# Performance work log

Hardware: AMD Instinct MI355X
Metric: run time of the kernel (lower is better)

## Reference

```python
import jax, jax.numpy as jnp
import numpy as np

DIM = 512
NUM_HEADS = 8
DIM_HEAD = 64
EPS = 1e-8
ROPE_THETA = 10000.0


def rms_norm(x, gamma):
    # F.normalize(x, dim=-1, p=2, eps) * sqrt(dim) * gamma
    norm = jnp.sqrt(jnp.sum(x * x, axis=-1, keepdims=True))
    x = x / jnp.maximum(norm, EPS)
    return x * (DIM ** 0.5) * gamma


def apply_rope(x):
    # x: [b, h, n, d], interleaved-pair RoPE (rotary-embedding-torch style)
    n, d = x.shape[-2], x.shape[-1]
    inv_freq = 1.0 / (ROPE_THETA ** (jnp.arange(0, d, 2, dtype=jnp.float32) / d))
    freqs = jnp.arange(n, dtype=jnp.float32)[:, None] * inv_freq[None, :]  # [n, d/2]
    freqs = jnp.repeat(freqs, 2, axis=-1)  # [n, d]
    cos, sin = jnp.cos(freqs), jnp.sin(freqs)
    x1 = x[..., ::2]
    x2 = x[..., 1::2]
    rot = jnp.stack((-x2, x1), axis=-1).reshape(x.shape)
    return x * cos + rot * sin


def setup_inputs() -> dict:
    key = jax.random.key(0)
    k1, k2, k3, k4 = jax.random.split(key, 4)
    b, n = 4, 2048
    dim_inner = NUM_HEADS * DIM_HEAD
    x = jax.random.normal(k1, (b, n, DIM), dtype=jnp.float32)
    gamma = jnp.ones((DIM,), dtype=jnp.float32)
    w_qkv = jax.random.normal(k2, (DIM, 3 * dim_inner), dtype=jnp.float32) * (DIM ** -0.5)
    w_out = jax.random.normal(k3, (dim_inner, DIM), dtype=jnp.float32) * (dim_inner ** -0.5)
    return {"x": x, "gamma": gamma, "w_qkv": w_qkv, "w_out": w_out}


def reference(x, gamma, w_qkv, w_out):
    b, n, _ = x.shape
    h, d = NUM_HEADS, DIM_HEAD
    xn = rms_norm(x, gamma)
    qkv = xn @ w_qkv  # [b, n, 3*h*d]
    qkv = qkv.reshape(b, n, 3, h, d)
    q = jnp.transpose(qkv[:, :, 0], (0, 2, 1, 3))  # [b, h, n, d]
    k = jnp.transpose(qkv[:, :, 1], (0, 2, 1, 3))
    v = jnp.transpose(qkv[:, :, 2], (0, 2, 1, 3))
    q = apply_rope(q)
    k = apply_rope(k)
    scale = d ** -0.5
    attn = jnp.einsum('bhnd,bhmd->bhnm', q, k) * scale
    attn = jax.nn.softmax(attn, axis=-1)
    out = jnp.einsum('bhnm,bhmd->bhnd', attn, v)
    out = jnp.transpose(out, (0, 2, 1, 3)).reshape(b, n, h * d)
    return out @ w_out
```

## Files before the change

### kernel.cpp

```cpp
#include <hip/hip_runtime.h>
#include <hip/hip_bf16.h>
#include <cmath>

#define B_SZ 4
#define N_SEQ 2048
#define DIM 512
#define NH 8
#define DH 64
#define QKV_N 1536
#define ROWS (B_SZ * N_SEQ)

typedef __bf16 bf16x8 __attribute__((ext_vector_type(8)));
typedef __bf16 bf16x4 __attribute__((ext_vector_type(4)));
typedef float  f32x4  __attribute__((ext_vector_type(4)));

#define GLOAD_LDS16(gp, lp)                                                     \
    __builtin_amdgcn_global_load_lds(                                           \
        (const __attribute__((address_space(1))) void*)(gp),                    \
        (__attribute__((address_space(3))) void*)(lp), 16, 0, 0)

#define MFMA_BF16 __builtin_amdgcn_mfma_f32_16x16x32_bf16

__global__ __launch_bounds__(64) void rmscast_kernel(const float* __restrict__ x,
                                                     const float* __restrict__ gamma,
                                                     __bf16* __restrict__ A) {
    int row = blockIdx.x;
    int t = threadIdx.x;
    const float4* xr = (const float4*)(x + (size_t)row * DIM);
    float4 a = xr[t];
    float4 b = xr[t + 64];
    float ss = a.x*a.x + a.y*a.y + a.z*a.z + a.w*a.w
             + b.x*b.x + b.y*b.y + b.z*b.z + b.w*b.w;
    #pragma unroll
    for (int off = 32; off > 0; off >>= 1) ss += __shfl_xor(ss, off, 64);
    float s = 22.62741699796952f / fmaxf(sqrtf(ss), 1e-8f);
    const float4* gr = (const float4*)gamma;
    float4 g1 = gr[t], g2 = gr[t + 64];
    bf16x4 o1 = { (__bf16)(a.x*g1.x*s), (__bf16)(a.y*g1.y*s),
                  (__bf16)(a.z*g1.z*s), (__bf16)(a.w*g1.w*s) };
    bf16x4 o2 = { (__bf16)(b.x*g2.x*s), (__bf16)(b.y*g2.y*s),
                  (__bf16)(b.z*g2.z*s), (__bf16)(b.w*g2.w*s) };
    *(bf16x4*)(A + (size_t)row * DIM + t * 4)       = o1;
    *(bf16x4*)(A + (size_t)row * DIM + 256 + t * 4) = o2;
}

__device__ __forceinline__ void tcast_tile(const float* __restrict__ W,
                                           __bf16* __restrict__ Wt,
                                           int K, int N, int n0, int k0, int t,
                                           float (*Ls)[68]) {
    const int tx = t & 15, ty = t >> 4;
    #pragma unroll
    for (int i = 0; i < 4; i++) {
        int k = ty + i * 16;
        float4 v = *(const float4*)&W[(size_t)(k0 + k) * N + n0 + tx * 4];
        *(float4*)&Ls[k][tx * 4] = v;
    }
    __syncthreads();
    const int nrow = t >> 2, seg = (t & 3) * 16;
    bf16x8 o0, o1;
    #pragma unroll
    for (int j = 0; j < 8; j++) o0[j] = (__bf16)Ls[seg + j][nrow];
    #pragma unroll
    for (int j = 0; j < 8; j++) o1[j] = (__bf16)Ls[seg + 8 + j][nrow];
    *(bf16x8*)&Wt[(size_t)(n0 + nrow) * K + k0 + seg]     = o0;
    *(bf16x8*)&Wt[(size_t)(n0 + nrow) * K + k0 + seg + 8] = o1;
}

__global__ __launch_bounds__(256) void tcast2_kernel(const float* __restrict__ w_qkv,
                                                     const float* __restrict__ w_out,
                                                     __bf16* __restrict__ Wqkvt,
                                                     __bf16* __restrict__ Woutt) {
    __shared__ float Ls[64][68];
    const int bx = blockIdx.x, k0 = blockIdx.y * 64, t = threadIdx.x;
    if (bx < 24) tcast_tile(w_qkv, Wqkvt, DIM, QKV_N, bx * 64, k0, t, Ls);
    else         tcast_tile(w_out, Woutt, DIM, DIM, (bx - 24) * 64, k0, t, Ls);
}

template <int N, typename OutT>
__global__ __launch_bounds__(256) void gemm_bf16_kernel(const __bf16* __restrict__ A,
                                                        const __bf16* __restrict__ Bt,
                                                        OutT* __restrict__ C) {
    __shared__ __bf16 As[128 * 32];
    __shared__ __bf16 Bs[128 * 32];
    const int t = threadIdx.x;
    const int lane = t & 63;
    const int w = t >> 6;
    const int l16 = lane & 15, quad = lane >> 4;
    const int wr = w >> 1, wc = w & 1;
    const int row0 = blockIdx.y * 128, col0 = blockIdx.x * 128;

    f32x4 acc[4][4] = {};

    const int r0a = t >> 2,         ks0 = (t & 3) * 8;
    const int r1a = (t + 256) >> 2, ks1 = (t & 3) * 8;

    for (int kt = 0; kt < DIM; kt += 32) {
        __syncthreads();
        GLOAD_LDS16(A  + (size_t)(row0 + r0a) * DIM + kt + ks0, As + t * 8);
        GLOAD_LDS16(A  + (size_t)(row0 + r1a) * DIM + kt + ks1, As + (t + 256) * 8);
        GLOAD_LDS16(Bt + (size_t)(col0 + r0a) * DIM + kt + ks0, Bs + t * 8);
        GLOAD_LDS16(Bt + (size_t)(col0 + r1a) * DIM + kt + ks1, Bs + (t + 256) * 8);
        __syncthreads();
        bf16x8 af[4], bfr[4];
        #pragma unroll
        for (int mi = 0; mi < 4; mi++)
            af[mi] = *(const bf16x8*)(As + (wr * 64 + mi * 16 + l16) * 32 + quad * 8);
        #pragma unroll
        for (int ni = 0; ni < 4; ni++)
            bfr[ni] = *(const bf16x8*)(Bs + (wc * 64 + ni * 16 + l16) * 32 + quad * 8);
        #pragma unroll
        for (int mi = 0; mi < 4; mi++)
            #pragma unroll
            for (int ni = 0; ni < 4; ni++)
                acc[mi][ni] = MFMA_BF16(af[mi], bfr[ni], acc[mi][ni], 0, 0, 0);
    }
    #pragma unroll
    for (int mi = 0; mi < 4; mi++) {
        #pragma unroll
        for (int ni = 0; ni < 4; ni++) {
            #pragma unroll
            for (int r = 0; r < 4; r++) {
                int m = row0 + wr * 64 + mi * 16 + quad * 4 + r;
                int n = col0 + wc * 64 + ni * 16 + l16;
                if constexpr (sizeof(OutT) == 4) {
                    C[(size_t)m * N + n] = acc[mi][ni][r];
                } else {
                    C[(size_t)m * N + n] = (__bf16)acc[mi][ni][r];
                }
            }
        }
    }
}

__global__ __launch_bounds__(256) void prep_kernel(const __bf16* __restrict__ qkvb,
                                                   __bf16* __restrict__ Qb,
                                                   __bf16* __restrict__ Kf,
                                                   __bf16* __restrict__ Vf) {
    const int bx = blockIdx.x;
    const int nt = bx & 31;
    const int bh = bx >> 5;
    const int b  = bh >> 3;
    const int h  = bh & 7;
    const int t  = threadIdx.x;
    const float QSCALE = 0.18033688011112042f;

    {
        const int r  = t >> 2;
        const int d0 = (t & 3) << 4;
        const int pos = nt * 64 + r;
        const __bf16* qp = qkvb + (size_t)(b * N_SEQ + pos) * QKV_N + h * DH + d0;

        union Pack { __bf16 h[16]; uint4 u[2]; };
        Pack qi, ki, qo, ko;
        qi.u[0] = ((const uint4*)qp)[0];         qi.u[1] = ((const uint4*)qp)[1];
        ki.u[0] = ((const uint4*)(qp + 512))[0]; ki.u[1] = ((const uint4*)(qp + 512))[1];

        #pragma unroll
        for (int i = 0; i < 8; i++) {
            int p = (d0 >> 1) + i;
            float inv = exp2f(-0.41524101186092028f * (float)p);
            float ang = (float)pos * inv;
            float sn, cs;
            sincosf(ang, &sn, &cs);
            float qe = (float)qi.h[2*i], qd = (float)qi.h[2*i+1];
            float ke = (float)ki.h[2*i], kd = (float)ki.h[2*i+1];
            qo.h[2*i]   = (__bf16)(QSCALE * (qe * cs - qd * sn));
            qo.h[2*i+1] = (__bf16)(QSCALE * (qd * cs + qe * sn));
            ko.h[2*i]   = (__bf16)(ke * cs - kd * sn);
            ko.h[2*i+1] = (__bf16)(kd * cs + ke * sn);
        }
        uint4* qd_ = (uint4*)(Qb + ((size_t)bh * N_SEQ + pos) * DH + d0);
        qd_[0] = qo.u[0]; qd_[1] = qo.u[1];
        const int group = r >> 4, kl = r & 15;
        const int c = d0 >> 5, quad = (d0 & 31) >> 3;
        __bf16* kdst = Kf + ((size_t)bh * 32 + nt) * 4096
                          + (group * 2 + c) * 512 + (quad * 16 + kl) * 8;
        *(uint4*)kdst         = ko.u[0];
        *(uint4*)(kdst + 128) = ko.u[1];
    }

    {
        const int w = t >> 6, lane = t & 63;
        union Pack { __bf16 h[16]; uint4 u[2]; };
        Pack v;
        #pragma unroll
        for (int j = 0; j < 16; j++) {
            int row = nt * 64 + w * 16 + j;
            v.h[j] = qkvb[(size_t)(b * N_SEQ + row) * QKV_N + 1024 + h * DH + lane];
        }
        const int ng = lane >> 4, vl = lane & 15;
        __bf16* vdst = Vf + ((size_t)bh * 32 + nt) * 4096
                          + (ng * 2 + (w >> 1)) * 512 + (((w & 1) * 2) * 16 + vl) * 8;
        *(uint4*)vdst         = v.u[0];
        *(uint4*)(vdst + 128) = v.u[1];
    }
}

__global__ __launch_bounds__(256, 2) void attn_mfma_kernel(const __bf16* __restrict__ Qb,
                                                           const __bf16* __restrict__ Kf,
                                                           const __bf16* __restrict__ Vf,
                                                           __bf16* __restrict__ attn) {
    __shared__ __bf16 kv[3][8192];
    __shared__ __bf16 plds[4][2][16][68];

    const int t    = threadIdx.x;
    const int w    = t >> 6;
    const int lane = t & 63;
    const int l16  = lane & 15;
    const int quad = lane >> 4;

    const int bx = blockIdx.x;
    const int bh = bx & 31;
    const int qc = bx >> 5;
    const int b  = bh >> 3;
    const int h  = bh & 7;

    const int qrow = qc * 128 + w * 32;
    const __bf16* Qh = Qb + ((size_t)bh * N_SEQ + qrow) * DH;
    const __bf16* Kt = Kf + (size_t)bh * 32 * 4096;
    const __bf16* Vt = Vf + (size_t)bh * 32 * 4096;

    bf16x8 qa[2][2];
    #pragma unroll
    for (int f = 0; f < 2; f++) {
        qa[f][0] = *(const bf16x8*)(Qh + (size_t)(f * 16 + l16) * DH + quad * 8);
        qa[f][1] = *(const bf16x8*)(Qh + (size_t)(f * 16 + l16) * DH + 32 + quad * 8);
    }

    bf16x8 ones;
    #pragma unroll
    for (int i = 0; i < 8; i++) ones[i] = (__bf16)1.0f;

    f32x4 O[2][4] = {};
    f32x4 L[2] = {};

    auto dma_tile = [&](int tt, int bb) {
        const __bf16* kss = Kt + (size_t)tt * 4096;
        const __bf16* vss = Vt + (size_t)tt * 4096;
        GLOAD_LDS16(kss + w * 512 + lane * 8,       &kv[bb][w * 512 + lane * 8]);
        GLOAD_LDS16(kss + (w + 4) * 512 + lane * 8, &kv[bb][(w + 4) * 512 + lane * 8]);
        GLOAD_LDS16(vss + w * 512 + lane * 8,       &kv[bb][4096 + w * 512 + lane * 8]);
        GLOAD_LDS16(vss + (w + 4) * 512 + lane * 8, &kv[bb][4096 + (w + 4) * 512 + lane * 8]);
    };

    dma_tile(0, 0);
    dma_tile(1, 1);
    int cur = 0;
    #pragma unroll 1
    for (int tt = 0; tt < 32; tt++) {
        if (tt < 31)
            asm volatile("s_waitcnt vmcnt(4)\n\ts_barrier" ::: "memory");
        else
            asm volatile("s_waitcnt vmcnt(0)\n\ts_barrier" ::: "memory");
        if (tt + 2 < 32) {
            int pf = cur + 2; if (pf >= 3) pf -= 3;
            dma_tile(tt + 2, pf);
        }

        const __bf16* kb = kv[cur];
        const __bf16* vb = kv[cur] + 4096;

        bf16x8 kf[4][2];
        #pragma unroll
        for (int g = 0; g < 4; g++)
            #pragma unroll
            for (int c = 0; c < 2; c++)
                kf[g][c] = *(const bf16x8*)(kb + (g * 2 + c) * 512 + lane * 8);
        bf16x8 vf[4][2];
        #pragma unroll
        for (int n = 0; n < 4; n++)
            #pragma unroll
            for (int kc = 0; kc < 2; kc++)
                vf[n][kc] = *(const bf16x8*)(vb + (n * 2 + kc) * 512 + lane * 8);

        #pragma unroll
        for (int f = 0; f < 2; f++) {
            f32x4 S[4];
            #pragma unroll
            for (int g = 0; g < 4; g++) {
                f32x4 z = {0, 0, 0, 0};
                z = MFMA_BF16(qa[f][0], kf[g][0], z, 0, 0, 0);
                z = MFMA_BF16(qa[f][1], kf[g][1], z, 0, 0, 0);
                S[g] = z;
            }
            #pragma unroll
            for (int g = 0; g < 4; g++)
                #pragma unroll
                for (int r = 0; r < 4; r++)
                    plds[w][f][quad * 4 + r][g * 16 + l16] = (__bf16)exp2f(S[g][r]);
        }
        asm volatile("s_waitcnt lgkmcnt(0)" ::: "memory");
        #pragma unroll
        for (int f = 0; f < 2; f++) {
            bf16x8 pa0 = *(const bf16x8*)&plds[w][f][l16][quad * 8];
            bf16x8 pa1 = *(const bf16x8*)&plds[w][f][l16][32 + quad * 8];
            #pragma unroll
            for (int n = 0; n < 4; n++) {
                O[f][n] = MFMA_BF16(pa0, vf[n][0], O[f][n], 0, 0, 0);
                O[f][n] = MFMA_BF16(pa1, vf[n][1], O[f][n], 0, 0, 0);
            }
            L[f] = MFMA_BF16(pa0, ones, L[f], 0, 0, 0);
            L[f] = MFMA_BF16(pa1, ones, L[f], 0, 0, 0);
        }
        cur = (cur == 2) ? 0 : cur + 1;
    }

    #pragma unroll
    for (int f = 0; f < 2; f++) {
        float inv[4];
        #pragma unroll
        for (int r = 0; r < 4; r++) inv[r] = 1.0f / L[f][r];
        #pragma unroll
        for (int n = 0; n < 4; n++)
            #pragma unroll
            for (int r = 0; r < 4; r++) {
                size_t row = (size_t)(b * N_SEQ + qrow + f * 16 + quad * 4 + r);
                attn[row * 512 + h * DH + n * 16 + l16] = (__bf16)(O[f][n][r] * inv[r]);
            }
    }
}

extern "C" void kernel_launch(void* const* d_in, const int* in_sizes, int n_in,
                              void* d_out, int out_size, void* d_ws, size_t ws_size,
                              hipStream_t stream) {
    const float* x     = (const float*)d_in[0];
    const float* gamma = (const float*)d_in[1];
    const float* w_qkv = (const float*)d_in[2];
    const float* w_out = (const float*)d_in[3];
    float* out = (float*)d_out;

    __bf16* Abf   = (__bf16*)d_ws;
    __bf16* Wqkvt = Abf + (size_t)ROWS * DIM;
    __bf16* Woutt = Wqkvt + (size_t)QKV_N * DIM;
    __bf16* qkvb  = Woutt + (size_t)DIM * DIM;
    __bf16* attnb = qkvb;
    __bf16* Qb    = qkvb + (size_t)ROWS * QKV_N;
    __bf16* Kf    = Qb + (size_t)NH * B_SZ * N_SEQ * DH;
    __bf16* Vf    = Kf + (size_t)NH * B_SZ * N_SEQ * DH;

    rmscast_kernel<<<ROWS, 64, 0, stream>>>(x, gamma, Abf);
    tcast2_kernel<<<dim3(32, 8), 256, 0, stream>>>(w_qkv, w_out, Wqkvt, Woutt);
    gemm_bf16_kernel<QKV_N, __bf16><<<dim3(QKV_N / 128, ROWS / 128), 256, 0, stream>>>(
        Abf, Wqkvt, qkvb);
    prep_kernel<<<1024, 256, 0, stream>>>(qkvb, Qb, Kf, Vf);
    attn_mfma_kernel<<<512, 256, 0, stream>>>(Qb, Kf, Vf, attnb);
    gemm_bf16_kernel<DIM, float><<<dim3(DIM / 128, ROWS / 128), 256, 0, stream>>>(
        attnb, Woutt, out);
}
```

Measured before the change: 187.7 us.

## Fuse RoPE and QKV layout scatter into QKV GEMM epilogue, precompute cos/sin table

Replaces the separate prep kernel with a QKV GEMM whose epilogue applies RoPE through a precomputed cos/sin table and scatters results directly into the Q, K-fragment and V-fragment layouts. This removes the intermediate qkv buffer write and reread, plus per-element sincos work. The attention kernel drops from triple to double buffering with two barriers per tile. The epilogue now does scattered 2-byte stores, which may be poorly coalesced, and the reduced buffering may expose more load latency.

Result: slower. 199.3 us (+6.2%).

```diff
diff --git a/kernel.cpp b/kernel.cpp
--- a/kernel.cpp
+++ b/kernel.cpp
@@ -20,6 +20,15 @@
         (__attribute__((address_space(3))) void*)(lp), 16, 0, 0)
 
 #define MFMA_BF16 __builtin_amdgcn_mfma_f32_16x16x32_bf16
+
+__global__ __launch_bounds__(256) void cs_kernel(float2* __restrict__ cs) {
+    int idx = blockIdx.x * 256 + threadIdx.x;
+    int pos = idx >> 5, p = idx & 31;
+    float ang = (float)pos * exp2f(-0.41524101186092028f * (float)p);
+    float sn, c;
+    sincosf(ang, &sn, &c);
+    cs[idx] = make_float2(c, sn);
+}
 
 __global__ __launch_bounds__(64) void rmscast_kernel(const float* __restrict__ x,
                                                      const float* __restrict__ gamma,
@@ -132,67 +141,85 @@
     }
 }
 
-__global__ __launch_bounds__(256) void prep_kernel(const __bf16* __restrict__ qkvb,
-                                                   __bf16* __restrict__ Qb,
-                                                   __bf16* __restrict__ Kf,
-                                                   __bf16* __restrict__ Vf) {
-    const int bx = blockIdx.x;
-    const int nt = bx & 31;
-    const int bh = bx >> 5;
-    const int b  = bh >> 3;
-    const int h  = bh & 7;
-    const int t  = threadIdx.x;
+__global__ __launch_bounds__(256) void gemm_qkv_kernel(const __bf16* __restrict__ A,
+                                                       const __bf16* __restrict__ Bt,
+                                                       const float2* __restrict__ cstab,
+                                                       __bf16* __restrict__ Qb,
+                                                       __bf16* __restrict__ Kf,
+                                                       __bf16* __restrict__ Vf) {
+    __shared__ __bf16 As[128 * 32];
+    __shared__ __bf16 Bs[128 * 32];
+    const int t = threadIdx.x;
+    const int lane = t & 63;
+    const int w = t >> 6;
+    const int l16 = lane & 15, quad = lane >> 4;
+    const int wr = w >> 1, wc = w & 1;
+    const int row0 = blockIdx.y * 128, col0 = blockIdx.x * 128;
+
+    f32x4 acc[4][4] = {};
+
+    const int r0a = t >> 2,         ks0 = (t & 3) * 8;
+    const int r1a = (t + 256) >> 2, ks1 = (t & 3) * 8;
+
+    for (int kt = 0; kt < DIM; kt += 32) {
+        __syncthreads();
+        GLOAD_LDS16(A  + (size_t)(row0 + r0a) * DIM + kt + ks0, As + t * 8);
+        GLOAD_LDS16(A  + (size_t)(row0 + r1a) * DIM + kt + ks1, As + (t + 256) * 8);
+        GLOAD_LDS16(Bt + (size_t)(col0 + r0a) * DIM + kt + ks0, Bs + t * 8);
+        GLOAD_LDS16(Bt + (size_t)(col0 + r1a) * DIM + kt + ks1, Bs + (t + 256) * 8);
+        __syncthreads();
+        bf16x8 af[4], bfr[4];
+        #pragma unroll
+        for (int mi = 0; mi < 4; mi++)
+            af[mi] = *(const bf16x8*)(As + (wr * 64 + mi * 16 + l16) * 32 + quad * 8);
+        #pragma unroll
+        for (int ni = 0; ni < 4; ni++)
+            bfr[ni] = *(const bf16x8*)(Bs + (wc * 64 + ni * 16 + l16) * 32 + quad * 8);
+        #pragma unroll
+        for (int mi = 0; mi < 4; mi++)
+            #pragma unroll
+            for (int ni = 0; ni < 4; ni++)
+                acc[mi][ni] = MFMA_BF16(af[mi], bfr[ni], acc[mi][ni], 0, 0, 0);
+    }
+
+    const int region = blockIdx.x >> 2;
     const float QSCALE = 0.18033688011112042f;
-
-    {
-        const int r  = t >> 2;
-        const int d0 = (t & 3) << 4;
-        const int pos = nt * 64 + r;
-        const __bf16* qp = qkvb + (size_t)(b * N_SEQ + pos) * QKV_N + h * DH + d0;
-
-        union Pack { __bf16 h[16]; uint4 u[2]; };
-        Pack qi, ki, qo, ko;
-        qi.u[0] = ((const uint4*)qp)[0];         qi.u[1] = ((const uint4*)qp)[1];
-        ki.u[0] = ((const uint4*)(qp + 512))[0]; ki.u[1] = ((const uint4*)(qp + 512))[1];
-
-        #pragma unroll
-        for (int i = 0; i < 8; i++) {
-            int p = (d0 >> 1) + i;
-            float inv = exp2f(-0.41524101186092028f * (float)p);
-            float ang = (float)pos * inv;
-            float sn, cs;
-            sincosf(ang, &sn, &cs);
-            float qe = (float)qi.h[2*i], qd = (float)qi.h[2*i+1];
-            float ke = (float)ki.h[2*i], kd = (float)ki.h[2*i+1];
-            qo.h[2*i]   = (__bf16)(QSCALE * (qe * cs - qd * sn));
-            qo.h[2*i+1] = (__bf16)(QSCALE * (qd * cs + qe * sn));
-            ko.h[2*i]   = (__bf16)(ke * cs - kd * sn);
-            ko.h[2*i+1] = (__bf16)(kd * cs + ke * sn);
-        }
-        uint4* qd_ = (uint4*)(Qb + ((size_t)bh * N_SEQ + pos) * DH + d0);
-        qd_[0] = qo.u[0]; qd_[1] = qo.u[1];
-        const int group = r >> 4, kl = r & 15;
-        const int c = d0 >> 5, quad = (d0 & 31) >> 3;
-        __bf16* kdst = Kf + ((size_t)bh * 32 + nt) * 4096
-                          + (group * 2 + c) * 512 + (quad * 16 + kl) * 8;
-        *(uint4*)kdst         = ko.u[0];
-        *(uint4*)(kdst + 128) = ko.u[1];
-    }
-
-    {
-        const int w = t >> 6, lane = t & 63;
-        union Pack { __bf16 h[16]; uint4 u[2]; };
-        Pack v;
-        #pragma unroll
-        for (int j = 0; j < 16; j++) {
-            int row = nt * 64 + w * 16 + j;
-            v.h[j] = qkvb[(size_t)(b * N_SEQ + row) * QKV_N + 1024 + h * DH + lane];
-        }
-        const int ng = lane >> 4, vl = lane & 15;
-        __bf16* vdst = Vf + ((size_t)bh * 32 + nt) * 4096
-                          + (ng * 2 + (w >> 1)) * 512 + (((w & 1) * 2) * 16 + vl) * 8;
-        *(uint4*)vdst         = v.u[0];
-        *(uint4*)(vdst + 128) = v.u[1];
+    #pragma unroll
+    for (int mi = 0; mi < 4; mi++) {
+        #pragma unroll
+        for (int r = 0; r < 4; r++) {
+            const int m   = row0 + wr * 64 + mi * 16 + quad * 4 + r;
+            const int bb  = m >> 11;
+            const int pos = m & (N_SEQ - 1);
+            const int nt  = pos >> 6;
+            #pragma unroll
+            for (int ni = 0; ni < 4; ni++) {
+                const int c  = col0 + wc * 64 + ni * 16 + l16;
+                const int d  = c & 63;
+                const int bh = bb * 8 + ((c >> 6) & 7);
+                float v = acc[mi][ni][r];
+                if (region == 2) {
+                    const int keyloc = pos & 63;
+                    Vf[((size_t)bh * 32 + nt) * 4096
+                       + ((d >> 4) * 2 + (keyloc >> 5)) * 512
+                       + ((((keyloc >> 3) & 3) * 16 + (d & 15)) * 8) + (keyloc & 7)]
+                        = (__bf16)v;
+                } else {
+                    float2 cssn = cstab[pos * 32 + (d >> 1)];
+                    float pr = __shfl_xor(v, 1);
+                    float o = (d & 1) ? (v * cssn.x + pr * cssn.y)
+                                      : (v * cssn.x - pr * cssn.y);
+                    if (region == 0) {
+                        Qb[((size_t)bh * N_SEQ + pos) * DH + d] = (__bf16)(o * QSCALE);
+                    } else {
+                        Kf[((size_t)bh * 32 + nt) * 4096
+                           + (((pos >> 4) & 3) * 2 + (d >> 5)) * 512
+                           + ((((d >> 3) & 3) * 16 + (pos & 15)) * 8) + (d & 7)]
+                            = (__bf16)o;
+                    }
+                }
+            }
+        }
     }
 }
 
@@ -200,7 +227,7 @@
                                                            const __bf16* __restrict__ Kf,
                                                            const __bf16* __restrict__ Vf,
                                                            __bf16* __restrict__ attn) {
-    __shared__ __bf16 kv[3][8192];
+    __shared__ __bf16 kv[2][8192];
     __shared__ __bf16 plds[4][2][16][68];
 
     const int t    = threadIdx.x;
@@ -244,18 +271,16 @@
     };
 
     dma_tile(0, 0);
-    dma_tile(1, 1);
-    int cur = 0;
-    #pragma unroll 1
     for (int tt = 0; tt < 32; tt++) {
-        if (tt < 31)
-            asm volatile("s_waitcnt vmcnt(4)\n\ts_barrier" ::: "memory");
-        else
-            asm volatile("s_waitcnt vmcnt(0)\n\ts_barrier" ::: "memory");
-        if (tt + 2 < 32) {
-            int pf = cur + 2; if (pf >= 3) pf -= 3;
-            dma_tile(tt + 2, pf);
-        }
+        const int cur = tt & 1;
+        __syncthreads();
+        if (tt + 1 < 32) {
+            dma_tile(tt + 1, cur ^ 1);
+            asm volatile("s_waitcnt vmcnt(4)" ::: "memory");
+        } else {
+            asm volatile("s_waitcnt vmcnt(0)" ::: "memory");
+        }
+        __syncthreads();
 
         const __bf16* kb = kv[cur];
         const __bf16* vb = kv[cur] + 4096;
@@ -302,7 +327,6 @@
             L[f] = MFMA_BF16(pa0, ones, L[f], 0, 0, 0);
             L[f] = MFMA_BF16(pa1, ones, L[f], 0, 0, 0);
         }
-        cur = (cur == 2) ? 0 : cur + 1;
     }
 
     #pragma unroll
@@ -330,19 +354,19 @@
     float* out = (float*)d_out;
 
     __bf16* Abf   = (__bf16*)d_ws;
+    __bf16* attnb = Abf;
     __bf16* Wqkvt = Abf + (size_t)ROWS * DIM;
     __bf16* Woutt = Wqkvt + (size_t)QKV_N * DIM;
-    __bf16* qkvb  = Woutt + (size_t)DIM * DIM;
-    __bf16* attnb = qkvb;
-    __bf16* Qb    = qkvb + (size_t)ROWS * QKV_N;
+    __bf16* Qb    = Woutt + (size_t)DIM * DIM;
     __bf16* Kf    = Qb + (size_t)NH * B_SZ * N_SEQ * DH;
     __bf16* Vf    = Kf + (size_t)NH * B_SZ * N_SEQ * DH;
-
+    float2* cstab = (float2*)(Vf + (size_t)NH * B_SZ * N_SEQ * DH);
+
+    cs_kernel<<<256, 256, 0, stream>>>(cstab);
     rmscast_kernel<<<ROWS, 64, 0, stream>>>(x, gamma, Abf);
     tcast2_kernel<<<dim3(32, 8), 256, 0, stream>>>(w_qkv, w_out, Wqkvt, Woutt);
-    gemm_bf16_kernel<QKV_N, __bf16><<<dim3(QKV_N / 128, ROWS / 128), 256, 0, stream>>>(
-        Abf, Wqkvt, qkvb);
-    prep_kernel<<<1024, 256, 0, stream>>>(qkvb, Qb, Kf, Vf);
+    gemm_qkv_kernel<<<dim3(QKV_N / 128, ROWS / 128), 256, 0, stream>>>(
+        Abf, Wqkvt, cstab, Qb, Kf, Vf);
     attn_mfma_kernel<<<512, 256, 0, stream>>>(Qb, Kf, Vf, attnb);
     gemm_bf16_kernel<DIM, float><<<dim3(DIM / 128, ROWS / 128), 256, 0, stream>>>(
         attnb, Woutt, out);
```

## Switch attention KV pipeline to double-buffered 128-key tiles with per-fragment P staging

Applied to the files above, without the earlier changes.

Replaces the triple-buffered 64-key KV pipeline with a double-buffered scheme that loads 128 keys per stage. This halves the number of loop iterations, but each iteration now uses two barriers instead of one. P staging shrinks to a single buffer per wave, with a wait and reload per query fragment, and exp2f becomes the raw hardware builtin. LDS use grows while pipeline depth drops to one tile ahead, so less of the load latency may be hidden.

Result: faster. 175.7 us (-6.4%).

```diff
diff --git a/kernel.cpp b/kernel.cpp
--- a/kernel.cpp
+++ b/kernel.cpp
@@ -200,8 +200,8 @@
                                                            const __bf16* __restrict__ Kf,
                                                            const __bf16* __restrict__ Vf,
                                                            __bf16* __restrict__ attn) {
-    __shared__ __bf16 kv[3][8192];
-    __shared__ __bf16 plds[4][2][16][68];
+    __shared__ __bf16 kv[2][16384];
+    __shared__ __bf16 plds[4][16][68];
 
     const int t    = threadIdx.x;
     const int w    = t >> 6;
@@ -235,74 +235,79 @@
     f32x4 L[2] = {};
 
     auto dma_tile = [&](int tt, int bb) {
-        const __bf16* kss = Kt + (size_t)tt * 4096;
-        const __bf16* vss = Vt + (size_t)tt * 4096;
-        GLOAD_LDS16(kss + w * 512 + lane * 8,       &kv[bb][w * 512 + lane * 8]);
-        GLOAD_LDS16(kss + (w + 4) * 512 + lane * 8, &kv[bb][(w + 4) * 512 + lane * 8]);
-        GLOAD_LDS16(vss + w * 512 + lane * 8,       &kv[bb][4096 + w * 512 + lane * 8]);
-        GLOAD_LDS16(vss + (w + 4) * 512 + lane * 8, &kv[bb][4096 + (w + 4) * 512 + lane * 8]);
+        const __bf16* kss = Kt + (size_t)tt * 8192;
+        const __bf16* vss = Vt + (size_t)tt * 8192;
+        #pragma unroll
+        for (int seg = 0; seg < 2; seg++) {
+            GLOAD_LDS16(kss + seg * 4096 + w * 512 + lane * 8,
+                        &kv[bb][seg * 4096 + w * 512 + lane * 8]);
+            GLOAD_LDS16(kss + seg * 4096 + (w + 4) * 512 + lane * 8,
+                        &kv[bb][seg * 4096 + (w + 4) * 512 + lane * 8]);
+            GLOAD_LDS16(vss + seg * 4096 + w * 512 + lane * 8,
+                        &kv[bb][8192 + seg * 4096 + w * 512 + lane * 8]);
+            GLOAD_LDS16(vss + seg * 4096 + (w + 4) * 512 + lane * 8,
+                        &kv[bb][8192 + seg * 4096 + (w + 4) * 512 + lane * 8]);
+        }
     };
 
     dma_tile(0, 0);
-    dma_tile(1, 1);
-    int cur = 0;
-    #pragma unroll 1
-    for (int tt = 0; tt < 32; tt++) {
-        if (tt < 31)
-            asm volatile("s_waitcnt vmcnt(4)\n\ts_barrier" ::: "memory");
-        else
-            asm volatile("s_waitcnt vmcnt(0)\n\ts_barrier" ::: "memory");
-        if (tt + 2 < 32) {
-            int pf = cur + 2; if (pf >= 3) pf -= 3;
-            dma_tile(tt + 2, pf);
-        }
-
-        const __bf16* kb = kv[cur];
-        const __bf16* vb = kv[cur] + 4096;
-
-        bf16x8 kf[4][2];
-        #pragma unroll
-        for (int g = 0; g < 4; g++)
-            #pragma unroll
-            for (int c = 0; c < 2; c++)
-                kf[g][c] = *(const bf16x8*)(kb + (g * 2 + c) * 512 + lane * 8);
-        bf16x8 vf[4][2];
-        #pragma unroll
-        for (int n = 0; n < 4; n++)
-            #pragma unroll
-            for (int kc = 0; kc < 2; kc++)
-                vf[n][kc] = *(const bf16x8*)(vb + (n * 2 + kc) * 512 + lane * 8);
-
-        #pragma unroll
-        for (int f = 0; f < 2; f++) {
-            f32x4 S[4];
-            #pragma unroll
-            for (int g = 0; g < 4; g++) {
-                f32x4 z = {0, 0, 0, 0};
-                z = MFMA_BF16(qa[f][0], kf[g][0], z, 0, 0, 0);
-                z = MFMA_BF16(qa[f][1], kf[g][1], z, 0, 0, 0);
-                S[g] = z;
+    for (int tt = 0; tt < 16; tt++) {
+        const int cur = tt & 1;
+        __syncthreads();
+        if (tt + 1 < 16) {
+            dma_tile(tt + 1, cur ^ 1);
+            asm volatile("s_waitcnt vmcnt(8)" ::: "memory");
+        } else {
+            asm volatile("s_waitcnt vmcnt(0)" ::: "memory");
+        }
+        __syncthreads();
+
+        #pragma unroll
+        for (int hh = 0; hh < 2; hh++) {
+            const __bf16* kb = kv[cur] + hh * 4096;
+            const __bf16* vb = kv[cur] + 8192 + hh * 4096;
+
+            bf16x8 kf[4][2];
+            #pragma unroll
+            for (int g = 0; g < 4; g++)
+                #pragma unroll
+                for (int c = 0; c < 2; c++)
+                    kf[g][c] = *(const bf16x8*)(kb + (g * 2 + c) * 512 + lane * 8);
+            bf16x8 vf[4][2];
+            #pragma unroll
+            for (int n = 0; n < 4; n++)
+                #pragma unroll
+                for (int kc = 0; kc < 2; kc++)
+                    vf[n][kc] = *(const bf16x8*)(vb + (n * 2 + kc) * 512 + lane * 8);
+
+            #pragma unroll
+            for (int f = 0; f < 2; f++) {
+                f32x4 S[4];
+                #pragma unroll
+                for (int g = 0; g < 4; g++) {
+                    f32x4 z = {0, 0, 0, 0};
+                    z = MFMA_BF16(qa[f][0], kf[g][0], z, 0, 0, 0);
+                    z = MFMA_BF16(qa[f][1], kf[g][1], z, 0, 0, 0);
+                    S[g] = z;
+                }
+                #pragma unroll
+                for (int g = 0; g < 4; g++)
+                    #pragma unroll
+                    for (int r = 0; r < 4; r++)
+                        plds[w][quad * 4 + r][g * 16 + l16] =
+                            (__bf16)__builtin_amdgcn_exp2f(S[g][r]);
+                asm volatile("s_waitcnt lgkmcnt(0)" ::: "memory");
+                bf16x8 pa0 = *(const bf16x8*)&plds[w][l16][quad * 8];
+                bf16x8 pa1 = *(const bf16x8*)&plds[w][l16][32 + quad * 8];
+                #pragma unroll
+                for (int n = 0; n < 4; n++) {
+                    O[f][n] = MFMA_BF16(pa0, vf[n][0], O[f][n], 0, 0, 0);
+                    O[f][n] = MFMA_BF16(pa1, vf[n][1], O[f][n], 0, 0, 0);
+                }
+                L[f] = MFMA_BF16(pa0, ones, L[f], 0, 0, 0);
+                L[f] = MFMA_BF16(pa1, ones, L[f], 0, 0, 0);
             }
-            #pragma unroll
-            for (int g = 0; g < 4; g++)
-                #pragma unroll
-                for (int r = 0; r < 4; r++)
-                    plds[w][f][quad * 4 + r][g * 16 + l16] = (__bf16)exp2f(S[g][r]);
-        }
-        asm volatile("s_waitcnt lgkmcnt(0)" ::: "memory");
-        #pragma unroll
-        for (int f = 0; f < 2; f++) {
-            bf16x8 pa0 = *(const bf16x8*)&plds[w][f][l16][quad * 8];
-            bf16x8 pa1 = *(const bf16x8*)&plds[w][f][l16][32 + quad * 8];
-            #pragma unroll
-            for (int n = 0; n < 4; n++) {
-                O[f][n] = MFMA_BF16(pa0, vf[n][0], O[f][n], 0, 0, 0);
-                O[f][n] = MFMA_BF16(pa1, vf[n][1], O[f][n], 0, 0, 0);
-            }
-            L[f] = MFMA_BF16(pa0, ones, L[f], 0, 0, 0);
-            L[f] = MFMA_BF16(pa1, ones, L[f], 0, 0, 0);
-        }
-        cur = (cur == 2) ? 0 : cur + 1;
+        }
     }
 
     #pragma unroll
```
